# Optimization experiments

Measured on AMD Instinct MI355X. Metric: run time of the kernel, lower is better.

Reference implementation:

```python
import jax, jax.numpy as jnp
import numpy as np

B, C, H, W = 256, 256, 16, 16   # batch, backbone channels, spatial (H*W = 256 = loop count)
E, NCLS = 128, 200              # opt.embed_size, opt.class_num

def _conv(x, w, stride, pad):
    # NCHW / OIHW conv, explicit torch-style symmetric padding
    return jax.lax.conv_general_dilated(x, w, (stride, stride), [(pad, pad), (pad, pad)],
                                        dimension_numbers=('NCHW', 'OIHW', 'NCHW'))

def _bn(x, s, b):
    # eval-mode BatchNorm folded to per-channel scale + shift
    return x * s[None, :, None, None] + b[None, :, None, None]

def setup_inputs() -> dict:
    key = jax.random.key(0)
    ks = jax.random.split(key, 12)
    f = lambda k, shape, scale: jax.random.normal(k, shape, jnp.float32) * scale
    bn_s = lambda k, n: 1.0 + 0.05 * jax.random.normal(k, (n,), jnp.float32)
    bn_b = lambda k, n: 0.05 * jax.random.normal(k, (n,), jnp.float32)
    return {
        'x': f(ks[0], (B, C, H, W), 1.0),
        'embed_w': f(ks[1], (E, C), 0.05),
        'embed_b': f(ks[2], (E,), 0.05),
        'b1_conv1': f(ks[3], (512, 256, 3, 3), 0.03),
        'b1_bn1_s': bn_s(jax.random.fold_in(key, 101), 512),
        'b1_bn1_b': bn_b(jax.random.fold_in(key, 102), 512),
        'b1_conv2': f(ks[4], (512, 512, 3, 3), 0.02),
        'b1_bn2_s': bn_s(jax.random.fold_in(key, 103), 512),
        'b1_bn2_b': bn_b(jax.random.fold_in(key, 104), 512),
        'b1_down_w': f(ks[5], (512, 256, 1, 1), 0.05),
        'b1_down_s': bn_s(jax.random.fold_in(key, 105), 512),
        'b1_down_b': bn_b(jax.random.fold_in(key, 106), 512),
        'b2_conv1': f(ks[6], (512, 512, 3, 3), 0.02),
        'b2_bn1_s': bn_s(jax.random.fold_in(key, 107), 512),
        'b2_bn1_b': bn_b(jax.random.fold_in(key, 108), 512),
        'b2_conv2': f(ks[7], (512, 512, 3, 3), 0.02),
        'b2_bn2_s': bn_s(jax.random.fold_in(key, 109), 512),
        'b2_bn2_b': bn_b(jax.random.fold_in(key, 110), 512),
        'head_w': f(ks[8], (NCLS, 512), 0.05),
    }

def reference(x, embed_w, embed_b,
              b1_conv1, b1_bn1_s, b1_bn1_b, b1_conv2, b1_bn2_s, b1_bn2_b,
              b1_down_w, b1_down_s, b1_down_b,
              b2_conv1, b2_bn1_s, b2_bn1_b, b2_conv2, b2_bn2_s, b2_bn2_b,
              head_w):
    # --- resblock = resnet layer4 (two BasicBlocks, 256->512, stride 2) ---
    y = jax.nn.relu(_bn(_conv(x, b1_conv1, 2, 1), b1_bn1_s, b1_bn1_b))
    y = _bn(_conv(y, b1_conv2, 1, 1), b1_bn2_s, b1_bn2_b)
    sc = _bn(_conv(x, b1_down_w, 2, 0), b1_down_s, b1_down_b)
    y = jax.nn.relu(y + sc)                              # [B,512,8,8]
    z = jax.nn.relu(_bn(_conv(y, b2_conv1, 1, 1), b2_bn1_s, b2_bn1_b))
    z = _bn(_conv(z, b2_conv2, 1, 1), b2_bn2_s, b2_bn2_b)
    z = jax.nn.relu(z + y)
    # --- class prediction: global avg pool + bias-free linear ---
    feat = jnp.mean(z, axis=(2, 3))                      # [B,512]
    prediction = feat @ head_w.T                         # [B,NCLS]
    # --- consistency: 1x1-conv embedding, then pairwise Gram + sigmoid ---
    emb = jnp.einsum('bchw,ec->behw', x, embed_w) + embed_b[None, :, None, None]
    emb = emb.reshape(B, E, H * W)                       # [B,E,256]
    inv_sqrt_e = jnp.float32(1.0 / np.sqrt(E))
    # vol[b,q,i] = sum_c emb[b,c,i]*emb[b,c,q] / sqrt(E)  (matches the 256-iter loop)
    vol = jax.nn.sigmoid(jnp.einsum('bei,beq->bqi', emb, emb) * inv_sqrt_e)
    return (prediction, vol)
```

## Files before the change

kernel.cpp:

```cpp
#include <hip/hip_runtime.h>


using short8 = __attribute__((ext_vector_type(8))) short;
using f32x4  = __attribute__((ext_vector_type(4))) float;
typedef unsigned short u16;
typedef unsigned int   u32;

#define MFMA(a,b,c) __builtin_amdgcn_mfma_f32_16x16x32_bf16((a),(b),(c),0,0,0)

__device__ __forceinline__ u16 f2b(float f){
    u32 u = __builtin_bit_cast(u32, f);
    u += 0x7FFFu + ((u >> 16) & 1u);
    return (u16)(u >> 16);
}
__device__ __forceinline__ float b2f(u16 h){
    u32 u = ((u32)h) << 16;
    return __builtin_bit_cast(float, u);
}
__device__ __forceinline__ u32 pack2(float a, float b){
    return (u32)f2b(a) | ((u32)f2b(b) << 16);
}
__device__ __forceinline__ float sigmoidf_(float v){
    return 1.0f / (1.0f + __expf(-v));
}

__global__ __launch_bounds__(256)
void prep_kernel(const float* __restrict__ w1, const float* __restrict__ s1,
                 const float* __restrict__ w2, const float* __restrict__ s2,
                 const float* __restrict__ w3, const float* __restrict__ s3,
                 const float* __restrict__ w4, const float* __restrict__ s4,
                 const float* __restrict__ wd, const float* __restrict__ sd,
                 const float* __restrict__ ew,
                 u16* __restrict__ wp1, u16* __restrict__ wp2,
                 u16* __restrict__ wp3, u16* __restrict__ wp4,
                 u16* __restrict__ wpd, u16* __restrict__ wpe)
{
    const int N2 = 9*16*512*40, N1 = 9*8*512*40, ND = 8*512*40, NE = 8*128*40;
    int t = blockIdx.x * 256 + threadIdx.x;
    if (t < N2) {
        int j = t % 40; int r = t / 40; int co = r & 511; int q = r >> 9;
        int cc = q & 15; int dydx = q >> 4;
        float v = (j < 32) ? w2[(co*512 + cc*32 + j)*9 + dydx] * s2[co] : 0.f;
        wp2[t] = f2b(v); return;
    }
    t -= N2;
    if (t < N2) {
        int j = t % 40; int r = t / 40; int co = r & 511; int q = r >> 9;
        int cc = q & 15; int dydx = q >> 4;
        float v = (j < 32) ? w3[(co*512 + cc*32 + j)*9 + dydx] * s3[co] : 0.f;
        wp3[t] = f2b(v); return;
    }
    t -= N2;
    if (t < N2) {
        int j = t % 40; int r = t / 40; int co = r & 511; int q = r >> 9;
        int cc = q & 15; int dydx = q >> 4;
        float v = (j < 32) ? w4[(co*512 + cc*32 + j)*9 + dydx] * s4[co] : 0.f;
        wp4[t] = f2b(v); return;
    }
    t -= N2;
    if (t < N1) {
        int j = t % 40; int r = t / 40; int co = r & 511; int q = r >> 9;
        int cc = q & 7; int dydx = q >> 3;
        float v = (j < 32) ? w1[(co*256 + cc*32 + j)*9 + dydx] * s1[co] : 0.f;
        wp1[t] = f2b(v); return;
    }
    t -= N1;
    if (t < ND) {
        int j = t % 40; int r = t / 40; int co = r & 511; int cc = r >> 9;
        float v = (j < 32) ? wd[co*256 + cc*32 + j] * sd[co] : 0.f;
        wpd[t] = f2b(v); return;
    }
    t -= ND;
    if (t < NE) {
        int j = t % 40; int r = t / 40; int e = r & 127; int cc = r >> 7;
        float v = (j < 32) ? ew[e*256 + cc*32 + j] : 0.f;
        wpe[t] = f2b(v);
    }
}

__global__ __launch_bounds__(512, 2)
void conv1_kernel(const float* __restrict__ x, const u16* __restrict__ wp,
                  const float* __restrict__ bnb, u16* __restrict__ out)
{
    const int cot = blockIdx.x;
    const int b0  = blockIdx.y * 2;
    const int tid = threadIdx.x;
    const int wid = tid >> 6, lane = tid & 63;
    const int ln = lane & 15, kg = lane >> 4;
    const int wco = wid >> 1;
    const int bb  = wid & 1;

    __shared__ u16 actb[2][2*289*40];

    {
        short8 zz = {0,0,0,0,0,0,0,0};
        short8* ab = (short8*)&actb[0][0];
        for (int j = tid; j < 2*2*289*40/8; j += 512) ab[j] = zz;
    }
    __syncthreads();

    auto stage_act = [&](int cc, int p){
        #pragma unroll
        for (int it = 0; it < 16; ++it){
            int f = it*512 + tid;
            int bb2 = f >> 12; int rem = f & 4095;
            int cip = rem >> 8; int px = rem & 255;
            const float* src = &x[(((size_t)(b0+bb2)*256 + cc*32 + 2*cip)*256) + px];
            float v0 = src[0], v1 = src[256];
            int r = ((px >> 4) + 1)*17 + (px & 15) + 1;
            *(u32*)&actb[p][(bb2*289 + r)*40 + 2*cip] = pack2(v0, v1);
        }
    };

    stage_act(0, 0);
    __syncthreads();

    f32x4 zero4 = {0.f,0.f,0.f,0.f};
    f32x4 acc[4][4];
    #pragma unroll
    for (int mf = 0; mf < 4; ++mf)
        #pragma unroll
        for (int nf = 0; nf < 4; ++nf) acc[mf][nf] = zero4;

    int bbase[4];
    #pragma unroll
    for (int nf = 0; nf < 4; ++nf){
        int px = nf*16 + ln;
        bbase[nf] = (bb*289 + 34*(px>>3) + 2*(px&7))*40 + kg*8;
    }

    for (int cc = 0; cc < 8; ++cc){
        if (cc < 7) stage_act(cc+1, (cc+1) & 1);
        const u16* abp = actb[cc & 1];
        #pragma unroll
        for (int d = 0; d < 9; ++d){
            const u16* wdp = wp + ((size_t)(d*8 + cc)*512 + cot*256)*40;
            int dy = d/3, dx = d - dy*3;
            int shift = (dy*17 + dx)*40;
            short8 A[4];
            #pragma unroll
            for (int mf = 0; mf < 4; ++mf)
                A[mf] = *(const short8*)&wdp[(wco*64 + mf*16 + ln)*40 + kg*8];
            #pragma unroll
            for (int nf = 0; nf < 4; ++nf){
                short8 B = *(const short8*)&abp[bbase[nf] + shift];
                #pragma unroll
                for (int mf = 0; mf < 4; ++mf)
                    acc[mf][nf] = MFMA(A[mf], B, acc[mf][nf]);
            }
        }
        __syncthreads();
    }

    #pragma unroll
    for (int mf = 0; mf < 4; ++mf){
        int co0 = cot*256 + wco*64 + mf*16 + kg*4;
        float4 bv = *(const float4*)&bnb[co0];
        #pragma unroll
        for (int nf = 0; nf < 4; ++nf){
            int px = nf*16 + ln;
            size_t o = (((size_t)(b0+bb)*64) + px)*512 + co0;
            f32x4 a = acc[mf][nf];
            ushort4 st;
            st.x = f2b(fmaxf(a[0] + bv.x, 0.f));
            st.y = f2b(fmaxf(a[1] + bv.y, 0.f));
            st.z = f2b(fmaxf(a[2] + bv.z, 0.f));
            st.w = f2b(fmaxf(a[3] + bv.w, 0.f));
            *(ushort4*)&out[o] = st;
        }
    }
}

template<int DOWN, int RES>
__global__ __launch_bounds__(64, 2)
void conv_s1_kernel(const u16* __restrict__ in, const u16* __restrict__ wp,
                    const float* __restrict__ bnb,
                    const float* __restrict__ x, const u16* __restrict__ wpd,
                    const float* __restrict__ dbb,
                    const u16* __restrict__ res, u16* __restrict__ out)
{
    const int b   = blockIdx.x;
    const int cot = blockIdx.y;
    const int lane = threadIdx.x;
    const int ln = lane & 15, kg = lane >> 4;

    __shared__ u16 actb[2][100*40];

    {
        short8 zz = {0,0,0,0,0,0,0,0};
        short8* ab = (short8*)&actb[0][0];
        #pragma unroll
        for (int it = 0; it < 16; ++it){
            int j = it*64 + lane;
            if (j < 1000) ab[j] = zz;
        }
    }

    int s_ld[4]; size_t s_go[4];
    #pragma unroll
    for (int it = 0; it < 4; ++it){
        int j = it*64 + lane;
        int px = j >> 2, cg = j & 3;
        int row = ((px>>3)+1)*10 + (px&7) + 1;
        s_ld[it] = row*40 + ((cg + row) % 5)*8;
        s_go[it] = (((size_t)b*64 + px)*512) + cg*8;
    }

    short8 sreg[4];
    auto stage_load = [&](int cc){
        #pragma unroll
        for (int it = 0; it < 4; ++it)
            sreg[it] = *(const short8*)&in[s_go[it] + cc*32];
    };
    auto stage_store = [&](int p){
        #pragma unroll
        for (int it = 0; it < 4; ++it)
            *(short8*)&actb[p][s_ld[it]] = sreg[it];
    };

    stage_load(0); stage_store(0);

    f32x4 zero4 = {0.f,0.f,0.f,0.f};
    f32x4 acc[4][4];
    #pragma unroll
    for (int mf = 0; mf < 4; ++mf)
        #pragma unroll
        for (int nf = 0; nf < 4; ++nf) acc[mf][nf] = zero4;

    int bro9[3][3][4];
    #pragma unroll
    for (int dy = 0; dy < 3; ++dy)
        #pragma unroll
        for (int dx = 0; dx < 3; ++dx)
            #pragma unroll
            for (int nf = 0; nf < 4; ++nf){
                int px = nf*16 + ln;
                int row = (px>>3)*10 + (px&7) + dy*10 + dx;
                bro9[dy][dx][nf] = row*40 + ((kg + row) % 5)*8;
            }

    const int aoff = ln*40 + kg*8;
    const int abase = cot*64*40;

    for (int cc = 0; cc < 16; ++cc){
        if (cc < 15) stage_load(cc+1);
        const u16* abp = actb[cc & 1];
        #pragma unroll
        for (int dy = 0; dy < 3; ++dy){
            short8 A[3][4];
            #pragma unroll
            for (int dx = 0; dx < 3; ++dx){
                const u16* wdp = wp + (size_t)((dy*3+dx)*16 + cc)*512*40 + abase;
                #pragma unroll
                for (int mf = 0; mf < 4; ++mf)
                    A[dx][mf] = *(const short8*)&wdp[mf*640 + aoff];
            }
            #pragma unroll
            for (int dx = 0; dx < 3; ++dx){
                #pragma unroll
                for (int nf = 0; nf < 4; ++nf){
                    short8 B = *(const short8*)&abp[bro9[dy][dx][nf]];
                    #pragma unroll
                    for (int mf = 0; mf < 4; ++mf)
                        acc[mf][nf] = MFMA(A[dx][mf], B, acc[mf][nf]);
                }
            }
        }
        if (cc < 15) stage_store((cc+1) & 1);
    }

    if (DOWN){
        for (int dc = 0; dc < 8; ++dc){
            #pragma unroll
            for (int it = 0; it < 16; ++it){
                int f = it*64 + lane;
                int cip = f >> 6, px2 = f & 63;
                int ipx = (px2>>3)*32 + (px2&7)*2;
                const float* src = &x[(((size_t)b*256 + dc*32 + 2*cip)*256) + ipx];
                int slot = ((cip>>2) + px2) % 5;
                *(u32*)&actb[0][px2*40 + slot*8 + (cip&3)*2] = pack2(src[0], src[256]);
            }
            const u16* wdp = wpd + (size_t)(dc*512)*40 + abase;
            short8 A[4];
            #pragma unroll
            for (int mf = 0; mf < 4; ++mf)
                A[mf] = *(const short8*)&wdp[mf*640 + aoff];
            #pragma unroll
            for (int nf = 0; nf < 4; ++nf){
                int rd = nf*16 + ln;
                short8 B = *(const short8*)&actb[0][rd*40 + ((kg + rd) % 5)*8];
                #pragma unroll
                for (int mf = 0; mf < 4; ++mf)
                    acc[mf][nf] = MFMA(A[mf], B, acc[mf][nf]);
            }
        }
    }

    #pragma unroll
    for (int mf = 0; mf < 4; ++mf){
        int co0 = cot*64 + mf*16 + kg*4;
        float4 bv = *(const float4*)&bnb[co0];
        if (DOWN){
            float4 dv = *(const float4*)&dbb[co0];
            bv.x += dv.x; bv.y += dv.y; bv.z += dv.z; bv.w += dv.w;
        }
        #pragma unroll
        for (int nf = 0; nf < 4; ++nf){
            int px = nf*16 + ln;
            size_t o = (((size_t)b*64) + px)*512 + co0;
            f32x4 a = acc[mf][nf];
            float v0 = a[0] + bv.x, v1 = a[1] + bv.y;
            float v2 = a[2] + bv.z, v3 = a[3] + bv.w;
            if (RES){
                ushort4 rv = *(const ushort4*)&res[o];
                v0 += b2f(rv.x); v1 += b2f(rv.y); v2 += b2f(rv.z); v3 += b2f(rv.w);
            }
            ushort4 st;
            st.x = f2b(fmaxf(v0, 0.f)); st.y = f2b(fmaxf(v1, 0.f));
            st.z = f2b(fmaxf(v2, 0.f)); st.w = f2b(fmaxf(v3, 0.f));
            *(ushort4*)&out[o] = st;
        }
    }
}

__global__ __launch_bounds__(256)
void head_kernel(const u16* __restrict__ z, const float* __restrict__ hw,
                 float* __restrict__ pred)
{
    const int b = blockIdx.x, tid = threadIdx.x;
    __shared__ float feat[512];
    float s0 = 0.f, s1 = 0.f;
    for (int px = 0; px < 64; ++px){
        u32 u = *(const u32*)&z[(((size_t)b*64 + px)*512) + 2*tid];
        s0 += b2f((u16)(u & 0xFFFF));
        s1 += b2f((u16)(u >> 16));
    }
    feat[2*tid]   = s0 * (1.f/64.f);
    feat[2*tid+1] = s1 * (1.f/64.f);
    __syncthreads();
    if (tid < 200){
        float acc = 0.f;
        const float4* hp = (const float4*)&hw[(size_t)tid*512];
        #pragma unroll 8
        for (int i = 0; i < 128; ++i){
            float4 h = hp[i];
            float4 f = *(const float4*)&feat[i*4];
            acc += h.x*f.x + h.y*f.y + h.z*f.z + h.w*f.w;
        }
        pred[b*200 + tid] = acc;
    }
}

__global__ __launch_bounds__(512, 2)
void gram_kernel(const float* __restrict__ x, const u16* __restrict__ wpe,
                 const float* __restrict__ eb, float* __restrict__ vol)
{
    const int b = blockIdx.x, tid = threadIdx.x;
    const int wid = tid >> 6, lane = tid & 63;
    const int ln = lane & 15, kg = lane >> 4;

    __shared__ u16 embl[256*136];
    __shared__ u16 xbl[256*40];
    __shared__ u16 ewl[128*40];

    f32x4 zero4 = {0.f,0.f,0.f,0.f};
    f32x4 ae[8][2];
    #pragma unroll
    for (int mf = 0; mf < 8; ++mf){ ae[mf][0] = zero4; ae[mf][1] = zero4; }

    for (int cc = 0; cc < 8; ++cc){
        __syncthreads();
        #pragma unroll
        for (int it = 0; it < 8; ++it){
            int f = it*512 + tid;
            int cip = f >> 8, px = f & 255;
            const float* src = &x[(((size_t)b*256 + cc*32 + 2*cip)*256) + px];
            *(u32*)&xbl[px*40 + 2*cip] = pack2(src[0], src[256]);
        }
        for (int j = tid; j < 640; j += 512)
            *(short8*)&ewl[j*8] = *(const short8*)&wpe[(cc*128)*40 + j*8];
        __syncthreads();
        short8 A[8];
        #pragma unroll
        for (int mf = 0; mf < 8; ++mf)
            A[mf] = *(const short8*)&ewl[(mf*16 + ln)*40 + kg*8];
        #pragma unroll
        for (int nf = 0; nf < 2; ++nf){
            short8 B = *(const short8*)&xbl[(wid*32 + nf*16 + ln)*40 + kg*8];
            #pragma unroll
            for (int mf = 0; mf < 8; ++mf)
                ae[mf][nf] = MFMA(A[mf], B, ae[mf][nf]);
        }
    }
    #pragma unroll
    for (int mf = 0; mf < 8; ++mf){
        int e0 = mf*16 + kg*4;
        float4 bv = *(const float4*)&eb[e0];
        #pragma unroll
        for (int nf = 0; nf < 2; ++nf){
            int px = wid*32 + nf*16 + ln;
            f32x4 a = ae[mf][nf];
            ushort4 st;
            st.x = f2b(a[0] + bv.x); st.y = f2b(a[1] + bv.y);
            st.z = f2b(a[2] + bv.z); st.w = f2b(a[3] + bv.w);
            *(ushort4*)&embl[px*136 + e0] = st;
        }
    }
    __syncthreads();

    const int wq = wid >> 2, wi = wid & 3;
    f32x4 g[8][4];
    #pragma unroll
    for (int mf = 0; mf < 8; ++mf)
        #pragma unroll
        for (int nf = 0; nf < 4; ++nf) g[mf][nf] = zero4;

    #pragma unroll
    for (int ks = 0; ks < 4; ++ks){
        short8 A[8];
        #pragma unroll
        for (int mf = 0; mf < 8; ++mf)
            A[mf] = *(const short8*)&embl[(wq*128 + mf*16 + ln)*136 + ks*32 + kg*8];
        #pragma unroll
        for (int nf = 0; nf < 4; ++nf){
            short8 B = *(const short8*)&embl[(wi*64 + nf*16 + ln)*136 + ks*32 + kg*8];
            #pragma unroll
            for (int mf = 0; mf < 8; ++mf)
                g[mf][nf] = MFMA(A[mf], B, g[mf][nf]);
        }
    }
    const float sc = 0.08838834764831845f;
    #pragma unroll
    for (int mf = 0; mf < 8; ++mf){
        #pragma unroll
        for (int nf = 0; nf < 4; ++nf){
            int i = wi*64 + nf*16 + ln;
            #pragma unroll
            for (int r = 0; r < 4; ++r){
                int q = wq*128 + mf*16 + kg*4 + r;
                vol[(((size_t)b*256 + q)*256) + i] = sigmoidf_(g[mf][nf][r] * sc);
            }
        }
    }
}

extern "C" void kernel_launch(void* const* d_in, const int* in_sizes, int n_in,
                              void* d_out, int out_size, void* d_ws, size_t ws_size,
                              hipStream_t stream)
{
    const float* x    = (const float*)d_in[0];
    const float* ew   = (const float*)d_in[1];
    const float* eb   = (const float*)d_in[2];
    const float* w1   = (const float*)d_in[3];
    const float* bn1s = (const float*)d_in[4];
    const float* bn1b = (const float*)d_in[5];
    const float* w2   = (const float*)d_in[6];
    const float* bn2s = (const float*)d_in[7];
    const float* bn2b = (const float*)d_in[8];
    const float* wd   = (const float*)d_in[9];
    const float* bnds = (const float*)d_in[10];
    const float* bndb = (const float*)d_in[11];
    const float* w3   = (const float*)d_in[12];
    const float* bn3s = (const float*)d_in[13];
    const float* bn3b = (const float*)d_in[14];
    const float* w4   = (const float*)d_in[15];
    const float* bn4s = (const float*)d_in[16];
    const float* bn4b = (const float*)d_in[17];
    const float* hw   = (const float*)d_in[18];

    float* pred = (float*)d_out;
    float* vol  = pred + 51200;

    u16* wp2 = (u16*)d_ws;
    u16* wp3 = wp2 + 2949120;
    u16* wp4 = wp3 + 2949120;
    u16* wp1 = wp4 + 2949120;
    u16* wpd = wp1 + 1474560;
    u16* wpe = wpd + 163840;

    u16* y1 = (u16*)vol;
    u16* y  = y1 + 8388608;
    u16* z1 = y  + 8388608;
    u16* z  = z1 + 8388608;

    prep_kernel<<<41120, 256, 0, stream>>>(w1, bn1s, w2, bn2s, w3, bn3s, w4, bn4s,
                                           wd, bnds, ew, wp1, wp2, wp3, wp4, wpd, wpe);
    conv1_kernel<<<dim3(2,128), 512, 0, stream>>>(x, wp1, bn1b, y1);
    conv_s1_kernel<1,0><<<dim3(256,8), 64, 0, stream>>>(y1, wp2, bn2b, x, wpd, bndb,
                                                        nullptr, y);
    conv_s1_kernel<0,0><<<dim3(256,8), 64, 0, stream>>>(y, wp3, bn3b, nullptr, nullptr,
                                                        nullptr, nullptr, z1);
    conv_s1_kernel<0,1><<<dim3(256,8), 64, 0, stream>>>(z1, wp4, bn4b, nullptr, nullptr,
                                                        nullptr, y, z);
    head_kernel<<<256, 256, 0, stream>>>(z, hw, pred);
    gram_kernel<<<256, 512, 0, stream>>>(x, wpe, eb, vol);
}
```

Baseline: 427.3 us.

## Use pre-padded global activations, drop LDS staging, fuse avg-pool into last conv

Intermediate activations are now stored in a zero-padded 10x10 spatial layout in global memory, so the 3x3 conv kernels read B operands straight from global or cache instead of staging them through double-buffered LDS with swizzling. A zero kernel clears the padded buffers once per call. The final residual conv also accumulates the global average pool with warp shuffles and writes a feature vector, so the z tensor is never stored and the head kernel only reads it. This removes LDS traffic and synchronisation but replaces it with repeated uncoalesced global loads (nine taps per channel chunk), which may stress L1/L2 bandwidth.

```diff
diff --git a/kernel.cpp b/kernel.cpp
--- a/kernel.cpp
+++ b/kernel.cpp
@@ -22,6 +22,15 @@
 }
 __device__ __forceinline__ float sigmoidf_(float v){
     return 1.0f / (1.0f + __expf(-v));
+}
+
+__global__ __launch_bounds__(256)
+void zero_kernel(short8* __restrict__ p, int n)
+{
+    short8 zz = {0,0,0,0,0,0,0,0};
+    int i = blockIdx.x * 256 + threadIdx.x;
+    int stride = gridDim.x * 256;
+    for (; i < n; i += stride) p[i] = zz;
 }
 
 __global__ __launch_bounds__(256)
@@ -159,7 +168,7 @@
         #pragma unroll
         for (int nf = 0; nf < 4; ++nf){
             int px = nf*16 + ln;
-            size_t o = (((size_t)(b0+bb)*64) + px)*512 + co0;
+            size_t o = ((size_t)(b0+bb)*100 + ((px>>3)+1)*10 + (px&7) + 1)*512 + co0;
             f32x4 a = acc[mf][nf];
             ushort4 st;
             st.x = f2b(fmaxf(a[0] + bv.x, 0.f));
@@ -171,54 +180,37 @@
     }
 }
 
-template<int DOWN, int RES>
+template<int DOWN, int RES, int GAP>
 __global__ __launch_bounds__(64, 2)
 void conv_s1_kernel(const u16* __restrict__ in, const u16* __restrict__ wp,
                     const float* __restrict__ bnb,
                     const float* __restrict__ x, const u16* __restrict__ wpd,
                     const float* __restrict__ dbb,
-                    const u16* __restrict__ res, u16* __restrict__ out)
+                    const u16* __restrict__ res, u16* __restrict__ out,
+                    float* __restrict__ feat)
 {
     const int b   = blockIdx.x;
     const int cot = blockIdx.y;
     const int lane = threadIdx.x;
     const int ln = lane & 15, kg = lane >> 4;
 
-    __shared__ u16 actb[2][100*40];
-
-    {
-        short8 zz = {0,0,0,0,0,0,0,0};
-        short8* ab = (short8*)&actb[0][0];
-        #pragma unroll
-        for (int it = 0; it < 16; ++it){
-            int j = it*64 + lane;
-            if (j < 1000) ab[j] = zz;
-        }
-    }
-
-    int s_ld[4]; size_t s_go[4];
-    #pragma unroll
-    for (int it = 0; it < 4; ++it){
-        int j = it*64 + lane;
-        int px = j >> 2, cg = j & 3;
-        int row = ((px>>3)+1)*10 + (px&7) + 1;
-        s_ld[it] = row*40 + ((cg + row) % 5)*8;
-        s_go[it] = (((size_t)b*64 + px)*512) + cg*8;
-    }
-
-    short8 sreg[4];
-    auto stage_load = [&](int cc){
-        #pragma unroll
-        for (int it = 0; it < 4; ++it)
-            sreg[it] = *(const short8*)&in[s_go[it] + cc*32];
-    };
-    auto stage_store = [&](int p){
-        #pragma unroll
-        for (int it = 0; it < 4; ++it)
-            *(short8*)&actb[p][s_ld[it]] = sreg[it];
-    };
-
-    stage_load(0); stage_store(0);
+    __shared__ u16 dbuf[64*40];
+
+    int boff[3][3][4];
+    #pragma unroll
+    for (int dy = 0; dy < 3; ++dy)
+        #pragma unroll
+        for (int dx = 0; dx < 3; ++dx)
+            #pragma unroll
+            for (int nf = 0; nf < 4; ++nf){
+                int px = nf*16 + ln;
+                int py = px >> 3, pxx = px & 7;
+                boff[dy][dx][nf] = (((py+dy)*10) + (pxx+dx))*512 + kg*8;
+            }
+
+    const u16* ab = in + (size_t)b*51200;
+    const int aoff = ln*40 + kg*8;
+    const int abase = cot*64*40;
 
     f32x4 zero4 = {0.f,0.f,0.f,0.f};
     f32x4 acc[4][4];
@@ -227,24 +219,8 @@
         #pragma unroll
         for (int nf = 0; nf < 4; ++nf) acc[mf][nf] = zero4;
 
-    int bro9[3][3][4];
-    #pragma unroll
-    for (int dy = 0; dy < 3; ++dy)
-        #pragma unroll
-        for (int dx = 0; dx < 3; ++dx)
-            #pragma unroll
-            for (int nf = 0; nf < 4; ++nf){
-                int px = nf*16 + ln;
-                int row = (px>>3)*10 + (px&7) + dy*10 + dx;
-                bro9[dy][dx][nf] = row*40 + ((kg + row) % 5)*8;
-            }
-
-    const int aoff = ln*40 + kg*8;
-    const int abase = cot*64*40;
-
     for (int cc = 0; cc < 16; ++cc){
-        if (cc < 15) stage_load(cc+1);
-        const u16* abp = actb[cc & 1];
+        const u16* abc = ab + cc*32;
         #pragma unroll
         for (int dy = 0; dy < 3; ++dy){
             short8 A[3][4];
@@ -259,14 +235,13 @@
             for (int dx = 0; dx < 3; ++dx){
                 #pragma unroll
                 for (int nf = 0; nf < 4; ++nf){
-                    short8 B = *(const short8*)&abp[bro9[dy][dx][nf]];
+                    short8 B = *(const short8*)&abc[boff[dy][dx][nf]];
                     #pragma unroll
                     for (int mf = 0; mf < 4; ++mf)
                         acc[mf][nf] = MFMA(A[dx][mf], B, acc[mf][nf]);
                 }
             }
         }
-        if (cc < 15) stage_store((cc+1) & 1);
     }
 
     if (DOWN){
@@ -277,8 +252,7 @@
                 int cip = f >> 6, px2 = f & 63;
                 int ipx = (px2>>3)*32 + (px2&7)*2;
                 const float* src = &x[(((size_t)b*256 + dc*32 + 2*cip)*256) + ipx];
-                int slot = ((cip>>2) + px2) % 5;
-                *(u32*)&actb[0][px2*40 + slot*8 + (cip&3)*2] = pack2(src[0], src[256]);
+                *(u32*)&dbuf[px2*40 + cip*2] = pack2(src[0], src[256]);
             }
             const u16* wdp = wpd + (size_t)(dc*512)*40 + abase;
             short8 A[4];
@@ -288,12 +262,20 @@
             #pragma unroll
             for (int nf = 0; nf < 4; ++nf){
                 int rd = nf*16 + ln;
-                short8 B = *(const short8*)&actb[0][rd*40 + ((kg + rd) % 5)*8];
+                short8 B = *(const short8*)&dbuf[rd*40 + kg*8];
                 #pragma unroll
                 for (int mf = 0; mf < 4; ++mf)
                     acc[mf][nf] = MFMA(A[mf], B, acc[mf][nf]);
             }
         }
+    }
+
+    float gs[4][4];
+    if (GAP){
+        #pragma unroll
+        for (int mf = 0; mf < 4; ++mf)
+            #pragma unroll
+            for (int r = 0; r < 4; ++r) gs[mf][r] = 0.f;
     }
 
     #pragma unroll
@@ -307,7 +289,8 @@
         #pragma unroll
         for (int nf = 0; nf < 4; ++nf){
             int px = nf*16 + ln;
-            size_t o = (((size_t)b*64) + px)*512 + co0;
+            int py = px >> 3, pxx = px & 7;
+            size_t o = ((size_t)b*100 + (py+1)*10 + pxx + 1)*512 + co0;
             f32x4 a = acc[mf][nf];
             float v0 = a[0] + bv.x, v1 = a[1] + bv.y;
             float v2 = a[2] + bv.z, v3 = a[3] + bv.w;
@@ -315,28 +298,43 @@
                 ushort4 rv = *(const ushort4*)&res[o];
                 v0 += b2f(rv.x); v1 += b2f(rv.y); v2 += b2f(rv.z); v3 += b2f(rv.w);
             }
-            ushort4 st;
-            st.x = f2b(fmaxf(v0, 0.f)); st.y = f2b(fmaxf(v1, 0.f));
-            st.z = f2b(fmaxf(v2, 0.f)); st.w = f2b(fmaxf(v3, 0.f));
-            *(ushort4*)&out[o] = st;
-        }
+            v0 = fmaxf(v0, 0.f); v1 = fmaxf(v1, 0.f);
+            v2 = fmaxf(v2, 0.f); v3 = fmaxf(v3, 0.f);
+            if (GAP){
+                gs[mf][0] += v0; gs[mf][1] += v1;
+                gs[mf][2] += v2; gs[mf][3] += v3;
+            } else {
+                ushort4 st;
+                st.x = f2b(v0); st.y = f2b(v1); st.z = f2b(v2); st.w = f2b(v3);
+                *(ushort4*)&out[o] = st;
+            }
+        }
+    }
+
+    if (GAP){
+        #pragma unroll
+        for (int mf = 0; mf < 4; ++mf)
+            #pragma unroll
+            for (int r = 0; r < 4; ++r){
+                float v = gs[mf][r];
+                v += __shfl_xor(v, 1, 16);
+                v += __shfl_xor(v, 2, 16);
+                v += __shfl_xor(v, 4, 16);
+                v += __shfl_xor(v, 8, 16);
+                if (ln == 0)
+                    feat[(size_t)b*512 + cot*64 + mf*16 + kg*4 + r] = v * (1.f/64.f);
+            }
     }
 }
 
 __global__ __launch_bounds__(256)
-void head_kernel(const u16* __restrict__ z, const float* __restrict__ hw,
+void head_kernel(const float* __restrict__ feat, const float* __restrict__ hw,
                  float* __restrict__ pred)
 {
     const int b = blockIdx.x, tid = threadIdx.x;
-    __shared__ float feat[512];
-    float s0 = 0.f, s1 = 0.f;
-    for (int px = 0; px < 64; ++px){
-        u32 u = *(const u32*)&z[(((size_t)b*64 + px)*512) + 2*tid];
-        s0 += b2f((u16)(u & 0xFFFF));
-        s1 += b2f((u16)(u >> 16));
-    }
-    feat[2*tid]   = s0 * (1.f/64.f);
-    feat[2*tid+1] = s1 * (1.f/64.f);
+    __shared__ float fl[512];
+    fl[tid]       = feat[(size_t)b*512 + tid];
+    fl[tid + 256] = feat[(size_t)b*512 + tid + 256];
     __syncthreads();
     if (tid < 200){
         float acc = 0.f;
@@ -344,7 +342,7 @@
         #pragma unroll 8
         for (int i = 0; i < 128; ++i){
             float4 h = hp[i];
-            float4 f = *(const float4*)&feat[i*4];
+            float4 f = *(const float4*)&fl[i*4];
             acc += h.x*f.x + h.y*f.y + h.z*f.z + h.w*f.w;
         }
         pred[b*200 + tid] = acc;
@@ -477,21 +475,22 @@
     u16* wp1 = wp4 + 2949120;
     u16* wpd = wp1 + 1474560;
     u16* wpe = wpd + 163840;
+    float* feat = (float*)(wpe + 40960);
 
     u16* y1 = (u16*)vol;
-    u16* y  = y1 + 8388608;
-    u16* z1 = y  + 8388608;
-    u16* z  = z1 + 8388608;
-
+    u16* yp = y1 + 13107200;
+    u16* z1 = y1;
+
+    zero_kernel<<<2048, 256, 0, stream>>>((short8*)y1, 3276800);
     prep_kernel<<<41120, 256, 0, stream>>>(w1, bn1s, w2, bn2s, w3, bn3s, w4, bn4s,
                                            wd, bnds, ew, wp1, wp2, wp3, wp4, wpd, wpe);
     conv1_kernel<<<dim3(2,128), 512, 0, stream>>>(x, wp1, bn1b, y1);
-    conv_s1_kernel<1,0><<<dim3(256,8), 64, 0, stream>>>(y1, wp2, bn2b, x, wpd, bndb,
-                                                        nullptr, y);
-    conv_s1_kernel<0,0><<<dim3(256,8), 64, 0, stream>>>(y, wp3, bn3b, nullptr, nullptr,
-                                                        nullptr, nullptr, z1);
-    conv_s1_kernel<0,1><<<dim3(256,8), 64, 0, stream>>>(z1, wp4, bn4b, nullptr, nullptr,
-                                                        nullptr, y, z);
-    head_kernel<<<256, 256, 0, stream>>>(z, hw, pred);
+    conv_s1_kernel<1,0,0><<<dim3(256,8), 64, 0, stream>>>(y1, wp2, bn2b, x, wpd, bndb,
+                                                          nullptr, yp, nullptr);
+    conv_s1_kernel<0,0,0><<<dim3(256,8), 64, 0, stream>>>(yp, wp3, bn3b, nullptr, nullptr,
+                                                          nullptr, nullptr, z1, nullptr);
+    conv_s1_kernel<0,1,1><<<dim3(256,8), 64, 0, stream>>>(z1, wp4, bn4b, nullptr, nullptr,
+                                                          nullptr, yp, nullptr, feat);
+    head_kernel<<<256, 256, 0, stream>>>(feat, hw, pred);
     gram_kernel<<<256, 512, 0, stream>>>(x, wpe, eb, vol);
 }
```

New measurement: 604.6 us. +41.5%, slower.
